# Kernel optimization log

Measured on AMD Instinct MI355X. Metric: run time of the kernel, lower is better.

The kernel has to match this reference:

```python
import jax, jax.numpy as jnp
import numpy as np

B, T, C = 2, 1024, 1024
H = 16
HS = C // H          # head size = 64
ROT = HS // 2        # partial rotary dims = 32
CTX = 1024           # ctx_len (T <= CTX)
FFN_H = 3 * 1024     # GeGLU hidden = 3 * n_ffn
LN_EPS = 1e-5


def setup_inputs():
    key = jax.random.key(0)
    ks = jax.random.split(key, 20)
    s = 0.02
    f32 = jnp.float32
    p = {}
    p["x"] = jax.random.normal(ks[0], (B, T, C), f32)
    p["ln1_w"] = jnp.ones((C,), f32); p["ln1_b"] = jnp.zeros((C,), f32)
    p["ln2_w"] = jnp.ones((C,), f32); p["ln2_b"] = jnp.zeros((C,), f32)
    p["Wq"] = jax.random.normal(ks[1], (C, C), f32) * s; p["bq"] = jnp.zeros((C,), f32)
    p["Wk"] = jax.random.normal(ks[2], (C, C), f32) * s; p["bk"] = jnp.zeros((C,), f32)
    p["Wv"] = jax.random.normal(ks[3], (C, C), f32) * s; p["bv"] = jnp.zeros((C,), f32)
    p["Wo"] = jax.random.normal(ks[4], (C, C), f32) * s; p["bo"] = jnp.zeros((C,), f32)
    p["time_w"] = 1.0 + 0.01 * jax.random.normal(ks[5], (H, CTX), f32)
    p["time_alpha"] = 1.0 + 0.01 * jax.random.normal(ks[6], (H, 1, CTX), f32)
    p["time_beta"] = 1.0 + 0.01 * jax.random.normal(ks[7], (H, CTX, 1), f32)
    p["time_gamma"] = 1.0 + 0.01 * jax.random.normal(ks[8], (CTX, 1), f32)
    p["mix_w"] = jnp.eye(H, dtype=f32) + 0.02 * jax.random.normal(ks[9], (H, H), f32)
    p["Wkg"] = jax.random.normal(ks[10], (C, FFN_H), f32) * s; p["bkg"] = jnp.zeros((FFN_H,), f32)
    p["Wvg"] = jax.random.normal(ks[11], (C, FFN_H), f32) * s; p["bvg"] = jnp.zeros((FFN_H,), f32)
    p["Wwg"] = jax.random.normal(ks[12], (FFN_H, C), f32) * s; p["bwg"] = jnp.zeros((C,), f32)
    return p


def _ln(x, w, b):
    m = jnp.mean(x, axis=-1, keepdims=True)
    v = jnp.mean((x - m) ** 2, axis=-1, keepdims=True)
    return (x - m) * jax.lax.rsqrt(v + LN_EPS) * w + b


def _time_shift_half(x):
    # ZeroPad2d((0,0,1,-1)) on the first C//2 channels: shift down by one step in time
    c = x.shape[-1]
    shifted = jnp.pad(x[:, :-1, : c // 2], ((0, 0), (1, 0), (0, 0)))
    return jnp.concatenate([shifted, x[:, :, c // 2 :]], axis=-1)


def _decay_w(time_w, time_alpha, time_beta):
    # Toeplitz trick: [H, CTX] -> circulant [H, CTX, CTX] of relative-time weights
    TT = CTX
    w = jnp.pad(time_w, ((0, 0), (0, TT)))                 # [H, 2TT]
    w = jnp.tile(w, (1, TT))[:, :-TT]                      # [H, 2TT*TT - TT]
    w = w.reshape(-1, TT, 2 * TT - 1)[:, :, TT - 1 :]      # [H, TT, TT]
    return w[:, :T, :T] * time_alpha[:, :, :T] * time_beta[:, :T, :]


def _rotate_half(x):
    x1, x2 = x[..., : x.shape[-1] // 2], x[..., x.shape[-1] // 2 :]
    return jnp.concatenate([-x2, x1], axis=-1)


def _apply_rotary(q, k):
    # q, k: [B, H, T, ROT]
    inv_freq = 1.0 / (10000.0 ** (jnp.arange(0, ROT, 2, dtype=jnp.float32) / ROT))
    t = jnp.arange(T, dtype=jnp.float32)
    freqs = t[:, None] * inv_freq[None, :]                 # [T, ROT//2]
    emb = jnp.concatenate([freqs, freqs], axis=-1)         # [T, ROT]
    cos, sin = jnp.cos(emb), jnp.sin(emb)
    q = q * cos + _rotate_half(q) * sin
    k = k * cos + _rotate_half(k) * sin
    return q, k


def _mha_pro(x, Wq, bq, Wk, bk, Wv, bv, Wo, bo,
             time_w, time_alpha, time_beta, time_gamma, mix_w):
    w = _decay_w(time_w, time_alpha, time_beta)            # [H, T, T]
    xs = _time_shift_half(x)
    q = (xs @ Wq + bq).reshape(B, T, H, HS).transpose(0, 2, 1, 3)
    k = (xs @ Wk + bk).reshape(B, T, H, HS).transpose(0, 2, 1, 3)
    v = (xs @ Wv + bv).reshape(B, T, H, HS).transpose(0, 2, 1, 3)
    qr, qp = q[..., :ROT], q[..., ROT:]
    kr, kp = k[..., :ROT], k[..., ROT:]
    qr, kr = _apply_rotary(qr, kr)
    q = jnp.concatenate([qr, qp], axis=-1)
    k = jnp.concatenate([kr, kp], axis=-1)
    att = jnp.einsum('bhqd,bhkd->bhqk', q, k) * (1.0 / np.sqrt(HS))
    causal = jnp.tril(jnp.ones((T, T), dtype=bool))
    att = jnp.where(causal, att, -jnp.inf)
    att = jax.nn.softmax(att, axis=-1)
    att = att * w                                          # learned time-decay reweighting
    att = jnp.einsum('oi,biqk->boqk', mix_w, att)          # 1x1 conv head mixing
    y = jnp.einsum('bhqk,bhkd->bhqd', att, v)
    y = y.transpose(0, 2, 1, 3).reshape(B, T, C)
    return (y @ Wo + bo) * time_gamma[:T, :]


def _geglu(x, Wkg, bkg, Wvg, bvg, Wwg, bwg):
    kk = x @ Wkg + bkg
    vv = x @ Wvg + bvg
    return (jax.nn.gelu(kk, approximate=False) * vv) @ Wwg + bwg


def _block(x, ln1_w, ln1_b, ln2_w, ln2_b, Wq, bq, Wk, bk, Wv, bv, Wo, bo,
           time_w, time_alpha, time_beta, time_gamma, mix_w,
           Wkg, bkg, Wvg, bvg, Wwg, bwg):
    x = x + _mha_pro(_ln(x, ln1_w, ln1_b), Wq, bq, Wk, bk, Wv, bv, Wo, bo,
                     time_w, time_alpha, time_beta, time_gamma, mix_w)
    x = x + _geglu(_ln(x, ln2_w, ln2_b), Wkg, bkg, Wvg, bvg, Wwg, bwg)
    return x


def reference(x, ln1_w, ln1_b, ln2_w, ln2_b, Wq, bq, Wk, bk, Wv, bv, Wo, bo,
              time_w, time_alpha, time_beta, time_gamma, mix_w,
              Wkg, bkg, Wvg, bvg, Wwg, bwg):
    return _block(x, ln1_w, ln1_b, ln2_w, ln2_b, Wq, bq, Wk, bk, Wv, bv, Wo, bo,
                  time_w, time_alpha, time_beta, time_gamma, mix_w,
                  Wkg, bkg, Wvg, bvg, Wwg, bwg)
```

## Files before the change

### kernel.cpp

```cpp
#include <hip/hip_runtime.h>
#include <cstdint>
#include <cstddef>
#include <cstdio>

#define B_   2
#define T_   1024
#define C_   1024
#define H_   16
#define HS_  64
#define FFN_ 3072

typedef __bf16   bf16x8 __attribute__((ext_vector_type(8)));
typedef float    f32x4  __attribute__((ext_vector_type(4)));
typedef float    f32x16 __attribute__((ext_vector_type(16)));
typedef uint16_t u16x8  __attribute__((ext_vector_type(8)));

__device__ __forceinline__ uint16_t f2bf(float f){
  uint32_t u = __float_as_uint(f);
  u += 0x7FFFu + ((u >> 16) & 1u);
  return (uint16_t)(u >> 16);
}
__device__ __forceinline__ float bf2f(uint16_t h){
  return __uint_as_float(((uint32_t)h) << 16);
}
__device__ __forceinline__ bf16x8 ldb8(const uint16_t* p){
  return __builtin_bit_cast(bf16x8, *reinterpret_cast<const u16x8*>(p));
}
__device__ __forceinline__ f32x4 mfma16(bf16x8 a, bf16x8 b, f32x4 c){
  return __builtin_amdgcn_mfma_f32_16x16x32_bf16(a, b, c, 0, 0, 0);
}

typedef __attribute__((address_space(1))) const uint32_t* gas_t;
typedef __attribute__((address_space(3))) uint32_t* las_t;
__device__ __forceinline__ void gl_lds16(const uint16_t* g, uint16_t* l){
  __builtin_amdgcn_global_load_lds((gas_t)g, (las_t)l, 16, 0, 0);
}

__global__ __launch_bounds__(256) void k_transpose(const float* __restrict__ in,
                                                   uint16_t* __restrict__ out,
                                                   int R, int Cc){
  __shared__ float tile[32][33];
  int c0 = blockIdx.x*32, r0 = blockIdx.y*32;
  int tx = threadIdx.x, ty = threadIdx.y;
  #pragma unroll
  for (int i=0;i<4;i++) tile[ty+i*8][tx] = in[(size_t)(r0+ty+i*8)*Cc + c0+tx];
  __syncthreads();
  #pragma unroll
  for (int i=0;i<4;i++) out[(size_t)(c0+ty+i*8)*R + r0+tx] = f2bf(tile[tx][ty+i*8]);
}

__global__ void k_bcat(const float* __restrict__ bq, const float* __restrict__ bk,
                       const float* __restrict__ bv, const float* __restrict__ bkg,
                       const float* __restrict__ bvg, float* __restrict__ out){
  int i = blockIdx.x*256 + threadIdx.x;
  float v;
  if      (i < 1024) v = bq[i];
  else if (i < 2048) v = bk[i-1024];
  else if (i < 3072) v = bv[i-2048];
  else if (i < 6144) v = bkg[i-3072];
  else               v = bvg[i-6144];
  out[i] = v;
}

template<int SHIFT>
__global__ __launch_bounds__(256) void k_ln(const float* __restrict__ in,
                                            const float* __restrict__ w,
                                            const float* __restrict__ bia,
                                            uint16_t* __restrict__ out){
  int row = blockIdx.x;
  int t = row & (T_-1);
  const float* xr = in + (size_t)row*C_;
  float4 v = reinterpret_cast<const float4*>(xr)[threadIdx.x];
  float s  = v.x+v.y+v.z+v.w;
  float s2 = v.x*v.x+v.y*v.y+v.z*v.z+v.w*v.w;
  #pragma unroll
  for (int o=1;o<64;o<<=1){ s += __shfl_xor(s,o); s2 += __shfl_xor(s2,o); }
  __shared__ float red[8];
  int lane = threadIdx.x & 63, wid = threadIdx.x >> 6;
  if (lane == 0){ red[wid] = s; red[4+wid] = s2; }
  __syncthreads();
  s  = red[0]+red[1]+red[2]+red[3];
  s2 = red[4]+red[5]+red[6]+red[7];
  float mean = s * (1.f/1024.f);
  float var  = s2 * (1.f/1024.f) - mean*mean;
  float rs   = rsqrtf(var + 1e-5f);
  float vals[4] = {v.x, v.y, v.z, v.w};
  #pragma unroll
  for (int j=0;j<4;j++){
    int cc = threadIdx.x*4 + j;
    float o_ = (vals[j]-mean)*rs*w[cc] + bia[cc];
    uint16_t ob = f2bf(o_);
    if (SHIFT){
      if (cc < 512){
        if (t < T_-1) out[(size_t)(row+1)*C_ + cc] = ob;
        if (t == 0)   out[(size_t)row*C_ + cc] = 0;
      } else {
        out[(size_t)row*C_ + cc] = ob;
      }
    } else {
      out[(size_t)row*C_ + cc] = ob;
    }
  }
}

enum { EPI_QKV=0, EPI_WO=2, EPI_BF16=3, EPI_FFN2=4 };

template<int EPI, int BN>
__global__ __launch_bounds__(256) void k_gemm2(
    const uint16_t* __restrict__ A, const uint16_t* __restrict__ Bt,
    const float* __restrict__ bias, void* __restrict__ outp,
    int M, int N, int K,
    const float* __restrict__ aux0, const float* __restrict__ aux1)
{
  __shared__ uint16_t As[128*32];
  __shared__ uint16_t Bs[BN*32];
  const int m0 = blockIdx.y*128, n0 = blockIdx.x*BN;
  const int tid = threadIdx.x;
  const int lane = tid & 63, wid = tid >> 6;
  const int wy = wid >> 1, wx = wid & 1;
  const int l16 = lane & 15, lr = lane >> 4;
  const int WN = BN/2;
  const int NW = BN/32;
  const f32x4 z = {0.f,0.f,0.f,0.f};
  f32x4 acc[4][NW];
  #pragma unroll
  for (int m=0;m<4;m++)
    #pragma unroll
    for (int n=0;n<NW;n++) acc[m][n] = z;
  const int srow = tid >> 2, scol = (tid & 3)*8;
  for (int k0 = 0; k0 < K; k0 += 32){
    gl_lds16(A + (size_t)(m0 + srow)*K      + k0 + scol, As + tid*8);
    gl_lds16(A + (size_t)(m0 + 64 + srow)*K + k0 + scol, As + 2048 + tid*8);
    gl_lds16(Bt + (size_t)(n0 + srow)*K     + k0 + scol, Bs + tid*8);
    if constexpr (BN == 128)
      gl_lds16(Bt + (size_t)(n0 + 64 + srow)*K + k0 + scol, Bs + 2048 + tid*8);
    __syncthreads();
    bf16x8 af[4], bfr[NW];
    #pragma unroll
    for (int m=0;m<4;m++) af[m] = ldb8(As + (wy*64 + m*16 + l16)*32 + lr*8);
    #pragma unroll
    for (int n=0;n<NW;n++) bfr[n] = ldb8(Bs + (wx*WN + n*16 + l16)*32 + lr*8);
    #pragma unroll
    for (int m=0;m<4;m++)
      #pragma unroll
      for (int n=0;n<NW;n++) acc[m][n] = mfma16(af[m], bfr[n], acc[m][n]);
    __syncthreads();
  }
  if constexpr (EPI == EPI_QKV){
    const float linvf = exp2f(-(float)l16 * 0.83048202f);
    #pragma unroll
    for (int m=0;m<4;m++){
      #pragma unroll
      for (int r=0;r<4;r++){
        int row = m0 + wy*64 + m*16 + lr*4 + r;
        int bb = row >> 10, t = row & 1023;
        int col0 = n0 + wx*32 + l16;
        float v0 = acc[m][0][r] + bias[col0];
        float v1 = acc[m][1][r] + bias[col0+16];
        int kind = col0 >> 10, hcol = col0 & 1023;
        int h = hcol >> 6, d0 = hcol & 63;
        if (kind < 2 && wx == 0){
          float sn, cs;
          __sincosf((float)t * linvf, &sn, &cs);
          float r0 = v0*cs - v1*sn;
          float r1 = v1*cs + v0*sn;
          v0 = r0; v1 = r1;
        }
        uint16_t* dst = (uint16_t*)outp + (size_t)kind*2097152;
        if (kind < 2){
          size_t basei = (((size_t)bb*16 + h)*1024 + t)*64;
          dst[basei + d0]      = f2bf(v0);
          dst[basei + d0 + 16] = f2bf(v1);
        } else {
          size_t basei = ((size_t)bb*16 + h)*65536;
          dst[basei + (size_t)d0*1024 + t]      = f2bf(v0);
          dst[basei + (size_t)(d0+16)*1024 + t] = f2bf(v1);
        }
      }
    }
  } else {
    #pragma unroll
    for (int m=0;m<4;m++){
      #pragma unroll
      for (int n=0;n<NW;n++){
        int col = n0 + wx*WN + n*16 + l16;
        float bc_ = bias ? bias[col] : 0.f;
        #pragma unroll
        for (int r=0;r<4;r++){
          int row = m0 + wy*64 + m*16 + lr*4 + r;
          float v = acc[m][n][r] + bc_;
          if constexpr (EPI == EPI_WO){
            int t = row & (T_-1);
            ((float*)outp)[(size_t)row*N + col] = aux1[(size_t)row*N + col] + v*aux0[t];
          } else if constexpr (EPI == EPI_BF16){
            ((uint16_t*)outp)[(size_t)row*N + col] = f2bf(v);
          } else {
            ((float*)outp)[(size_t)row*N + col] = aux0[(size_t)row*N + col] + v;
          }
        }
      }
    }
  }
}

__global__ __launch_bounds__(256) void k_stats(const uint16_t* __restrict__ q,
                                               const uint16_t* __restrict__ kmat,
                                               float* __restrict__ sm, float* __restrict__ sl){
  int bh = blockIdx.x, qb = blockIdx.y;
  int lane = threadIdx.x & 63, wid = threadIdx.x >> 6;
  int l16 = lane & 15, lr = lane >> 4;
  int r0 = qb*64 + wid*16;
  const uint16_t* qh = q    + (size_t)bh*T_*HS_;
  const uint16_t* kh = kmat + (size_t)bh*T_*HS_;
  int kq = lr*8;
  bf16x8 a0 = ldb8(qh + (size_t)(r0 + l16)*HS_ + kq);
  bf16x8 a1 = ldb8(qh + (size_t)(r0 + l16)*HS_ + kq + 32);
  float m_[4], l_[4]; int rows[4];
  #pragma unroll
  for (int r=0;r<4;r++){ m_[r] = -1e30f; l_[r] = 0.f; rows[r] = r0 + lr*4 + r; }
  int ktmax = (r0 + 15) >> 4;
  for (int kt = 0; kt <= ktmax; kt++){
    bf16x8 b0 = ldb8(kh + (size_t)(kt*16 + l16)*HS_ + kq);
    bf16x8 b1 = ldb8(kh + (size_t)(kt*16 + l16)*HS_ + kq + 32);
    f32x4 s = {0.f,0.f,0.f,0.f};
    s = mfma16(a0, b0, s);
    s = mfma16(a1, b1, s);
    int kcol = kt*16 + l16;
    #pragma unroll
    for (int r=0;r<4;r++){
      float sv = (kcol <= rows[r]) ? s[r]*0.125f : -3.0e38f;
      float mn = fmaxf(m_[r], sv);
      l_[r] = l_[r]*__expf(m_[r] - mn) + __expf(sv - mn);
      m_[r] = mn;
    }
  }
  #pragma unroll
  for (int o=1;o<16;o<<=1){
    #pragma unroll
    for (int r=0;r<4;r++){
      float mo = __shfl_xor(m_[r], o);
      float lo = __shfl_xor(l_[r], o);
      float mn = fmaxf(m_[r], mo);
      l_[r] = l_[r]*__expf(m_[r] - mn) + lo*__expf(mo - mn);
      m_[r] = mn;
    }
  }
  if (l16 == 0){
    #pragma unroll
    for (int r=0;r<4;r++){
      sm[(size_t)bh*T_ + rows[r]] = m_[r];
      sl[(size_t)bh*T_ + rows[r]] = l_[r];
    }
  }
}

__global__ __launch_bounds__(512, 4) void k_attn(
    const uint16_t* __restrict__ q, const uint16_t* __restrict__ kmat,
    const uint16_t* __restrict__ vT,
    const float* __restrict__ sm, const float* __restrict__ sl,
    const float* __restrict__ tw, const float* __restrict__ alpha,
    const float* __restrict__ beta, const float* __restrict__ mixw,
    uint16_t* __restrict__ py)
{
  int qt = blockIdx.x, kc = blockIdx.y, b = blockIdx.z;
  if (8*kc > qt) return;
  const int q0 = qt*16, ck0 = kc*128;
  const int lc = min(127, q0 + 15 - ck0);
  const int nt = (lc >> 5) + 1;

  __shared__ uint32_t U32[8*512];
  __shared__ uint16_t Cm[16*520];
  __shared__ uint16_t TWL[16*160];

  const int tid = threadIdx.x;
  const int lane = tid & 63;
  const int wid = __builtin_amdgcn_readfirstlane(tid >> 6);
  const int l16 = lane & 15, lr = lane >> 4;
  const int l32 = lane & 31, g32 = lane >> 5;

  const int base = 1008 - q0 + ck0;
  for (int i = tid; i < 16*144; i += 512){
    int h = i / 144, t = i - h*144;
    int gi = base + t;
    TWL[h*160 + t] = (gi <= 1023) ? f2bf(tw[h*1024 + gi]) : (uint16_t)0;
  }

  float SM[2][4], BSL[2][4];
  bf16x8 qa[2][2];
  #pragma unroll
  for (int h2=0; h2<2; ++h2){
    int h = 2*wid + h2, bh = b*16 + h;
    float4 s4 = *reinterpret_cast<const float4*>(sm   + (size_t)bh*1024 + q0 + lr*4);
    float4 l4 = *reinterpret_cast<const float4*>(sl   + (size_t)bh*1024 + q0 + lr*4);
    float4 b4 = *reinterpret_cast<const float4*>(beta + (size_t)h*1024  + q0 + lr*4);
    SM[h2][0]=s4.x; SM[h2][1]=s4.y; SM[h2][2]=s4.z; SM[h2][3]=s4.w;
    BSL[h2][0]=b4.x/l4.x; BSL[h2][1]=b4.y/l4.y; BSL[h2][2]=b4.z/l4.z; BSL[h2][3]=b4.w/l4.w;
    #pragma unroll
    for (int kk=0;kk<2;kk++)
      qa[h2][kk] = ldb8(q + ((size_t)bh*1024 + q0 + l16)*64 + kk*32 + lr*8);
  }
  bf16x8 mwf;
  {
    u16x8 t8;
    #pragma unroll
    for (int j=0;j<8;j++){
      float v = (l32 < 16) ? mixw[l32*16 + g32*8 + j] : 0.f;
      t8[j] = f2bf(v);
    }
    mwf = __builtin_bit_cast(bf16x8, t8);
  }

  const f32x4 z = {0.f,0.f,0.f,0.f};
  f32x4 acc[2][4];
  #pragma unroll
  for (int oo=0;oo<2;oo++) for (int n=0;n<4;n++) acc[oo][n] = z;

  __syncthreads();

  for (int t = 0; t < nt; ++t){
    const int k0 = ck0 + t*32;
    f32x4 s[2][2];
    s[0][0]=z; s[0][1]=z; s[1][0]=z; s[1][1]=z;
    #pragma unroll
    for (int h2=0;h2<2;h2++){
      const uint16_t* kh = kmat + ((size_t)(b*16 + 2*wid + h2)*1024 + k0)*64;
      #pragma unroll
      for (int kk=0;kk<2;kk++){
        bf16x8 kb0 = ldb8(kh + (size_t)(l16)*64      + kk*32 + lr*8);
        bf16x8 kb1 = ldb8(kh + (size_t)(16 + l16)*64 + kk*32 + lr*8);
        s[h2][0] = mfma16(qa[h2][kk], kb0, s[h2][0]);
        s[h2][1] = mfma16(qa[h2][kk], kb1, s[h2][1]);
      }
    }
    #pragma unroll
    for (int n=0;n<2;n++){
      int kloc = n*16 + l16;
      int kg = k0 + kloc;
      float al0 = alpha[(2*wid+0)*1024 + kg];
      float al1 = alpha[(2*wid+1)*1024 + kg];
      #pragma unroll
      for (int r=0;r<4;r++){
        int qloc = lr*4 + r;
        bool ok = (kg <= q0 + qloc);
        int twi = 15 - qloc + (kg - ck0);
        float u0 = 0.f, u1 = 0.f;
        if (ok){
          u0 = __expf(s[0][n][r]*0.125f - SM[0][r]) * BSL[0][r] * al0 * bf2f(TWL[(2*wid+0)*160 + twi]);
          u1 = __expf(s[1][n][r]*0.125f - SM[1][r]) * BSL[1][r] * al1 * bf2f(TWL[(2*wid+1)*160 + twi]);
        }
        uint32_t pk = (uint32_t)f2bf(u0) | ((uint32_t)f2bf(u1) << 16);
        U32[wid*512 + qloc*32 + ((kloc + 8*(qloc>>2)) & 31)] = pk;
      }
    }
    __syncthreads();
    #pragma unroll
    for (int cc=0; cc<2; ++cc){
      int qrow = wid*2 + cc;
      int pbase = qrow*32;
      int swz = (l32 + 8*(qrow>>2)) & 31;
      u16x8 a8;
      uint32_t* a32 = reinterpret_cast<uint32_t*>(&a8);
      #pragma unroll
      for (int j=0;j<4;j++)
        a32[j] = U32[(4*g32 + j)*512 + pbase + swz];
      bf16x8 a = __builtin_bit_cast(bf16x8, a8);
      f32x16 zz{};
      f32x16 dd = __builtin_amdgcn_mfma_f32_32x32x16_bf16(a, mwf, zz, 0, 0, 0);
      if (l32 < 16){
        int o = l32;
        #pragma unroll
        for (int rg=0; rg<4; ++rg){
          int p0 = pbase + rg*8 + g32*4;
          uint32_t w0 = (uint32_t)f2bf(dd[4*rg+0]) | ((uint32_t)f2bf(dd[4*rg+1]) << 16);
          uint32_t w1 = (uint32_t)f2bf(dd[4*rg+2]) | ((uint32_t)f2bf(dd[4*rg+3]) << 16);
          uint2 pk2; pk2.x = w0; pk2.y = w1;
          *reinterpret_cast<uint2*>(Cm + (size_t)o*520 + p0) = pk2;
        }
      }
    }
    __syncthreads();
    #pragma unroll
    for (int oo=0;oo<2;oo++){
      int o = 2*wid + oo;
      bf16x8 cf = ldb8(Cm + (size_t)o*520 + l16*32 + lr*8);
      const uint16_t* vh = vT + (size_t)(b*16 + o)*64*1024;
      #pragma unroll
      for (int n=0;n<4;n++){
        bf16x8 vf = ldb8(vh + (size_t)(n*16 + l16)*1024 + k0 + lr*8);
        acc[oo][n] = mfma16(cf, vf, acc[oo][n]);
      }
    }
  }

  uint16_t* po = py + (((size_t)(b*64 + qt))*8 + kc)*16384;
  #pragma unroll
  for (int oo=0;oo<2;oo++){
    int o = 2*wid + oo;
    #pragma unroll
    for (int n=0;n<4;n++)
      #pragma unroll
      for (int r=0;r<4;r++){
        int qloc = lr*4 + r;
        po[o*1024 + qloc*64 + n*16 + l16] = f2bf(acc[oo][n][r]);
      }
  }
}

__global__ void k_yred(const uint16_t* __restrict__ py, uint16_t* __restrict__ y){
  int idx = blockIdx.x*256 + threadIdx.x;
  int d8 = idx & 7, qq = (idx>>3)&15, o = (idx>>7)&15, qt = (idx>>11)&63, b = idx>>17;
  int nch = (qt>>3) + 1;
  const uint16_t* p0 = py + (((size_t)(b*64+qt))*8)*16384 + o*1024 + qq*64 + d8*8;
  float s[8] = {0,0,0,0,0,0,0,0};
  for (int kc=0; kc<nch; kc++){
    u16x8 v = *reinterpret_cast<const u16x8*>(p0 + (size_t)kc*16384);
    #pragma unroll
    for (int e=0;e<8;e++) s[e] += bf2f(v[e]);
  }
  int t = qt*16 + qq;
  u16x8 w;
  #pragma unroll
  for (int e=0;e<8;e++) w[e] = f2bf(s[e]);
  *reinterpret_cast<u16x8*>(y + ((size_t)(b*1024 + t))*1024 + o*64 + d8*8) = w;
}

__global__ void k_geglu(const uint16_t* __restrict__ ffu, uint16_t* __restrict__ g){
  int i = blockIdx.x*256 + threadIdx.x;
  int row = i / 384, j8 = i - row*384;
  const uint16_t* pa = ffu + (size_t)row*6144 + j8*8;
  u16x8 a = *reinterpret_cast<const u16x8*>(pa);
  u16x8 b = *reinterpret_cast<const u16x8*>(pa + 3072);
  u16x8 o;
  #pragma unroll
  for (int e=0;e<8;e++){
    float xv = bf2f(a[e]);
    float gl = 0.5f*xv*(1.f + erff(xv*0.70710678118f));
    o[e] = f2bf(gl * bf2f(b[e]));
  }
  *reinterpret_cast<u16x8*>(g + (size_t)row*3072 + j8*8) = o;
}

extern "C" void kernel_launch(void* const* d_in, const int* in_sizes, int n_in,
                              void* d_out, int out_size, void* d_ws, size_t ws_size,
                              hipStream_t stream)
{
  const float* x      = (const float*)d_in[0];
  const float* ln1w   = (const float*)d_in[1];
  const float* ln1b   = (const float*)d_in[2];
  const float* ln2w   = (const float*)d_in[3];
  const float* ln2b   = (const float*)d_in[4];
  const float* Wq     = (const float*)d_in[5];
  const float* bq     = (const float*)d_in[6];
  const float* Wk     = (const float*)d_in[7];
  const float* bk     = (const float*)d_in[8];
  const float* Wv     = (const float*)d_in[9];
  const float* bv     = (const float*)d_in[10];
  const float* Wo     = (const float*)d_in[11];
  const float* bo     = (const float*)d_in[12];
  const float* tw     = (const float*)d_in[13];
  const float* talpha = (const float*)d_in[14];
  const float* tbeta  = (const float*)d_in[15];
  const float* tgamma = (const float*)d_in[16];
  const float* mixw   = (const float*)d_in[17];
  const float* Wkg    = (const float*)d_in[18];
  const float* bkg    = (const float*)d_in[19];
  const float* Wvg    = (const float*)d_in[20];
  const float* bvg    = (const float*)d_in[21];
  const float* Wwg    = (const float*)d_in[22];
  const float* bwg    = (const float*)d_in[23];

  char* ws = (char*)d_ws;
  size_t off = 0;
  auto alloc = [&](size_t bytes)->char*{
    char* p = ws + off; off += (bytes + 255) & ~(size_t)255; return p;
  };
  uint16_t* WqT  = (uint16_t*)alloc((size_t)C_*C_*2);
  uint16_t* WkT  = (uint16_t*)alloc((size_t)C_*C_*2);
  uint16_t* WvT  = (uint16_t*)alloc((size_t)C_*C_*2);
  uint16_t* WoT  = (uint16_t*)alloc((size_t)C_*C_*2);
  uint16_t* WkgT = (uint16_t*)alloc((size_t)FFN_*C_*2);
  uint16_t* WvgT = (uint16_t*)alloc((size_t)FFN_*C_*2);
  uint16_t* WwgT = (uint16_t*)alloc((size_t)C_*FFN_*2);
  uint16_t* xs   = (uint16_t*)alloc((size_t)B_*T_*C_*2);
  uint16_t* qbuf = (uint16_t*)alloc((size_t)B_*T_*C_*2);
  uint16_t* kbuf = (uint16_t*)alloc((size_t)B_*T_*C_*2);
  uint16_t* vT   = (uint16_t*)alloc((size_t)B_*T_*C_*2);
  float*    sm   = (float*)alloc((size_t)B_*H_*T_*4);
  float*    sl   = (float*)alloc((size_t)B_*H_*T_*4);
  uint16_t* ybuf = (uint16_t*)alloc((size_t)B_*T_*C_*2);
  float*    x1   = (float*)alloc((size_t)B_*T_*C_*4);
  float*    bcat = (float*)alloc((size_t)9216*4);
  char*     region = alloc((size_t)64*1024*1024);
  uint16_t* py  = (uint16_t*)region;
  uint16_t* ffu = (uint16_t*)region;
  uint16_t* gb  = (uint16_t*)(region + (size_t)2048*6144*2);

  if (off > ws_size){
    fprintf(stderr, "kernel_launch: ws too small (%zu needed, %zu given)\n", off, ws_size);
    return;
  }

  dim3 blk(256);
  dim3 tblk(32,8);
  k_transpose<<<dim3(32,32), tblk, 0, stream>>>(Wq,  WqT,  C_,  C_);
  k_transpose<<<dim3(32,32), tblk, 0, stream>>>(Wk,  WkT,  C_,  C_);
  k_transpose<<<dim3(32,32), tblk, 0, stream>>>(Wv,  WvT,  C_,  C_);
  k_transpose<<<dim3(32,32), tblk, 0, stream>>>(Wo,  WoT,  C_,  C_);
  k_transpose<<<dim3(96,32), tblk, 0, stream>>>(Wkg, WkgT, C_,  FFN_);
  k_transpose<<<dim3(96,32), tblk, 0, stream>>>(Wvg, WvgT, C_,  FFN_);
  k_transpose<<<dim3(32,96), tblk, 0, stream>>>(Wwg, WwgT, FFN_, C_);
  k_bcat<<<36, blk, 0, stream>>>(bq, bk, bv, bkg, bvg, bcat);

  k_ln<1><<<B_*T_, blk, 0, stream>>>(x, ln1w, ln1b, xs);

  k_gemm2<EPI_QKV,64><<<dim3(48,16), blk, 0, stream>>>(xs, WqT, bcat, qbuf, 2048, 3072, 1024, nullptr, nullptr);

  k_stats<<<dim3(B_*H_, T_/64), blk, 0, stream>>>(qbuf, kbuf, sm, sl);
  k_attn<<<dim3(64,8,B_), dim3(512), 0, stream>>>(qbuf, kbuf, vT, sm, sl,
                                                  tw, talpha, tbeta, mixw, py);
  k_yred<<<1024, blk, 0, stream>>>(py, ybuf);

  k_gemm2<EPI_WO,64><<<dim3(16,16), blk, 0, stream>>>(ybuf, WoT, bo, x1, 2048, 1024, 1024, tgamma, x);

  k_ln<0><<<B_*T_, blk, 0, stream>>>(x1, ln2w, ln2b, xs);

  k_gemm2<EPI_BF16,128><<<dim3(48,16), blk, 0, stream>>>(xs, WkgT, bcat+3072, ffu, 2048, 6144, 1024, nullptr, nullptr);
  k_geglu<<<3072, blk, 0, stream>>>(ffu, gb);
  k_gemm2<EPI_FFN2,64><<<dim3(16,16), blk, 0, stream>>>(gb, WwgT, bwg, d_out, 2048, 1024, 3072, x1, nullptr);
}
```

Measured before the change: 293.7 us.

## Prefetch V and alpha early in attention, raise MFMA priority, widen QKV tiles

The attention loop now issues the V-fragment and alpha global loads at the top of each iteration, so their latency overlaps the QK^T MFMAs and the softmax-weight computation. s_setprio is raised around the MFMA groups in both the GEMM and the attention kernel. The QKV projection switches to BN=128 tiles (half as many blocks), and its epilogue is generalized so each wave covers a full 64-wide head slice, with rotary applied to the first two 16-column fragments. This trades more registers and fewer blocks for better latency hiding.

```diff
diff --git a/kernel.cpp b/kernel.cpp
--- a/kernel.cpp
+++ b/kernel.cpp
@@ -140,13 +140,18 @@
     for (int m=0;m<4;m++) af[m] = ldb8(As + (wy*64 + m*16 + l16)*32 + lr*8);
     #pragma unroll
     for (int n=0;n<NW;n++) bfr[n] = ldb8(Bs + (wx*WN + n*16 + l16)*32 + lr*8);
+    __builtin_amdgcn_s_setprio(1);
     #pragma unroll
     for (int m=0;m<4;m++)
       #pragma unroll
       for (int n=0;n<NW;n++) acc[m][n] = mfma16(af[m], bfr[n], acc[m][n]);
+    __builtin_amdgcn_s_setprio(0);
     __syncthreads();
   }
   if constexpr (EPI == EPI_QKV){
+    const int colb = n0 + wx*WN;
+    const int kind = colb >> 10;
+    const int h = (colb >> 6) & 15;
     const float linvf = exp2f(-(float)l16 * 0.83048202f);
     #pragma unroll
     for (int m=0;m<4;m++){
@@ -154,27 +159,24 @@
       for (int r=0;r<4;r++){
         int row = m0 + wy*64 + m*16 + lr*4 + r;
         int bb = row >> 10, t = row & 1023;
-        int col0 = n0 + wx*32 + l16;
-        float v0 = acc[m][0][r] + bias[col0];
-        float v1 = acc[m][1][r] + bias[col0+16];
-        int kind = col0 >> 10, hcol = col0 & 1023;
-        int h = hcol >> 6, d0 = hcol & 63;
-        if (kind < 2 && wx == 0){
+        float v[NW];
+        #pragma unroll
+        for (int n=0;n<NW;n++) v[n] = acc[m][n][r] + bias[colb + n*16 + l16];
+        if (kind < 2){
           float sn, cs;
           __sincosf((float)t * linvf, &sn, &cs);
-          float r0 = v0*cs - v1*sn;
-          float r1 = v1*cs + v0*sn;
-          v0 = r0; v1 = r1;
-        }
-        uint16_t* dst = (uint16_t*)outp + (size_t)kind*2097152;
-        if (kind < 2){
+          float r0 = v[0]*cs - v[1]*sn;
+          float r1 = v[1]*cs + v[0]*sn;
+          v[0] = r0; v[1] = r1;
+          uint16_t* dst = (uint16_t*)outp + (size_t)kind*2097152;
           size_t basei = (((size_t)bb*16 + h)*1024 + t)*64;
-          dst[basei + d0]      = f2bf(v0);
-          dst[basei + d0 + 16] = f2bf(v1);
+          #pragma unroll
+          for (int n=0;n<NW;n++) dst[basei + n*16 + l16] = f2bf(v[n]);
         } else {
+          uint16_t* dst = (uint16_t*)outp + (size_t)2*2097152;
           size_t basei = ((size_t)bb*16 + h)*65536;
-          dst[basei + (size_t)d0*1024 + t]      = f2bf(v0);
-          dst[basei + (size_t)(d0+16)*1024 + t] = f2bf(v1);
+          #pragma unroll
+          for (int n=0;n<NW;n++) dst[basei + (size_t)(n*16 + l16)*1024 + t] = f2bf(v[n]);
         }
       }
     }
@@ -319,6 +321,21 @@
 
   for (int t = 0; t < nt; ++t){
     const int k0 = ck0 + t*32;
+    bf16x8 vf[2][4];
+    #pragma unroll
+    for (int oo=0;oo<2;oo++){
+      const uint16_t* vh = vT + (size_t)(b*16 + 2*wid + oo)*65536;
+      #pragma unroll
+      for (int n=0;n<4;n++)
+        vf[oo][n] = ldb8(vh + (size_t)(n*16 + l16)*1024 + k0 + lr*8);
+    }
+    float al[2][2];
+    #pragma unroll
+    for (int n=0;n<2;n++){
+      int kg = k0 + n*16 + l16;
+      al[0][n] = alpha[(2*wid+0)*1024 + kg];
+      al[1][n] = alpha[(2*wid+1)*1024 + kg];
+    }
     f32x4 s[2][2];
     s[0][0]=z; s[0][1]=z; s[1][0]=z; s[1][1]=z;
     #pragma unroll
@@ -328,16 +345,16 @@
       for (int kk=0;kk<2;kk++){
         bf16x8 kb0 = ldb8(kh + (size_t)(l16)*64      + kk*32 + lr*8);
         bf16x8 kb1 = ldb8(kh + (size_t)(16 + l16)*64 + kk*32 + lr*8);
+        __builtin_amdgcn_s_setprio(1);
         s[h2][0] = mfma16(qa[h2][kk], kb0, s[h2][0]);
         s[h2][1] = mfma16(qa[h2][kk], kb1, s[h2][1]);
+        __builtin_amdgcn_s_setprio(0);
       }
     }
     #pragma unroll
     for (int n=0;n<2;n++){
       int kloc = n*16 + l16;
       int kg = k0 + kloc;
-      float al0 = alpha[(2*wid+0)*1024 + kg];
-      float al1 = alpha[(2*wid+1)*1024 + kg];
       #pragma unroll
       for (int r=0;r<4;r++){
         int qloc = lr*4 + r;
@@ -345,8 +362,8 @@
         int twi = 15 - qloc + (kg - ck0);
         float u0 = 0.f, u1 = 0.f;
         if (ok){
-          u0 = __expf(s[0][n][r]*0.125f - SM[0][r]) * BSL[0][r] * al0 * bf2f(TWL[(2*wid+0)*160 + twi]);
-          u1 = __expf(s[1][n][r]*0.125f - SM[1][r]) * BSL[1][r] * al1 * bf2f(TWL[(2*wid+1)*160 + twi]);
+          u0 = __expf(s[0][n][r]*0.125f - SM[0][r]) * BSL[0][r] * al[0][n] * bf2f(TWL[(2*wid+0)*160 + twi]);
+          u1 = __expf(s[1][n][r]*0.125f - SM[1][r]) * BSL[1][r] * al[1][n] * bf2f(TWL[(2*wid+1)*160 + twi]);
         }
         uint32_t pk = (uint32_t)f2bf(u0) | ((uint32_t)f2bf(u1) << 16);
         U32[wid*512 + qloc*32 + ((kloc + 8*(qloc>>2)) & 31)] = pk;
@@ -365,7 +382,9 @@
         a32[j] = U32[(4*g32 + j)*512 + pbase + swz];
       bf16x8 a = __builtin_bit_cast(bf16x8, a8);
       f32x16 zz{};
+      __builtin_amdgcn_s_setprio(1);
       f32x16 dd = __builtin_amdgcn_mfma_f32_32x32x16_bf16(a, mwf, zz, 0, 0, 0);
+      __builtin_amdgcn_s_setprio(0);
       if (l32 < 16){
         int o = l32;
         #pragma unroll
@@ -383,12 +402,11 @@
     for (int oo=0;oo<2;oo++){
       int o = 2*wid + oo;
       bf16x8 cf = ldb8(Cm + (size_t)o*520 + l16*32 + lr*8);
-      const uint16_t* vh = vT + (size_t)(b*16 + o)*64*1024;
-      #pragma unroll
-      for (int n=0;n<4;n++){
-        bf16x8 vf = ldb8(vh + (size_t)(n*16 + l16)*1024 + k0 + lr*8);
-        acc[oo][n] = mfma16(cf, vf, acc[oo][n]);
-      }
+      __builtin_amdgcn_s_setprio(1);
+      #pragma unroll
+      for (int n=0;n<4;n++)
+        acc[oo][n] = mfma16(cf, vf[oo][n], acc[oo][n]);
+      __builtin_amdgcn_s_setprio(0);
     }
   }
 
@@ -513,7 +531,7 @@
 
   k_ln<1><<<B_*T_, blk, 0, stream>>>(x, ln1w, ln1b, xs);
 
-  k_gemm2<EPI_QKV,64><<<dim3(48,16), blk, 0, stream>>>(xs, WqT, bcat, qbuf, 2048, 3072, 1024, nullptr, nullptr);
+  k_gemm2<EPI_QKV,128><<<dim3(24,16), blk, 0, stream>>>(xs, WqT, bcat, qbuf, 2048, 3072, 1024, nullptr, nullptr);
 
   k_stats<<<dim3(B_*H_, T_/64), blk, 0, stream>>>(qbuf, kbuf, sm, sl);
   k_attn<<<dim3(64,8,B_), dim3(512), 0, stream>>>(qbuf, kbuf, vT, sm, sl,
```

Result: slower. 344.0 us (+17.1%).
